# Performance work log

Measured on AMD Instinct MI355X. Metric: run time of the kernel, lower is better.

## Reference

```python
import jax, jax.numpy as jnp
import numpy as np
from jax.scipy.special import logsumexp

DEPTH = 7
LOG_EPS = jnp.float32(-64.0)
EPS = jnp.float32(np.exp(-64.0))


def leaf_interval(depth, start_idx=0):
    if depth == 0:
        return ([start_idx], [start_idx], [], start_idx)
    l_l, l_r, l_adj, last = leaf_interval(depth - 1, start_idx)
    my = last + 1
    r_l, r_r, r_adj, last = leaf_interval(depth - 1, my + 1)
    return ([my] + l_l, [my] + r_r,
            [(l, r) for l in l_r for r in r_l] + l_adj + r_adj, last)


_start, _end, _adj, _ = leaf_interval(DEPTH)
_out_idx = np.array([i for i, _ in _adj], dtype=np.int32)
OUT_UNIQ, OUT_INV = np.unique(_out_idx, return_inverse=True)
IN_IDX = np.array([j for _, j in _adj], dtype=np.int32)
START_IDXS = np.array(_start, dtype=np.int32)
END_IDXS = np.array(_end, dtype=np.int32)
N_STATES = 2 ** (DEPTH + 1) - 1  # 255


def log_safe(x):
    m = x < EPS
    return jnp.where(m, LOG_EPS, jnp.log(jnp.where(m, EPS, x)))


def exp_safe(x):
    m = x < LOG_EPS
    return jnp.where(m, EPS, jnp.exp(jnp.where(m, LOG_EPS, x)))


def setup_inputs() -> dict:
    key = jax.random.key(0)
    k1, k2, k3 = jax.random.split(key, 3)
    V, B, vocab, T = N_STATES, 64, 5000, 50
    log_probs = jax.nn.log_softmax(
        jax.random.normal(k1, (V, B, vocab), dtype=jnp.float32), axis=-1)
    targets = jax.random.randint(k2, (T, B), 0, vocab)
    target_lengths = jax.random.randint(k3, (B,), 1, T + 1)
    return {"log_probs": log_probs, "targets": targets,
            "target_lengths": target_lengths}


def _forward_ctreec(extracted, target_lengths):
    # extracted: [T, B, V] time-major per-state label log-probs
    T, B, V = extracted.shape
    out_uniq = jnp.asarray(OUT_UNIQ)
    out_inv = jnp.asarray(OUT_INV)
    in_idx = jnp.asarray(IN_IDX)
    end_idxs = jnp.asarray(END_IDXS)
    prev0 = jnp.zeros((B, V), jnp.float32).at[:, jnp.asarray(START_IDXS)].set(1.0)
    acc0 = jnp.zeros((B,), jnp.float32)

    def step(carry, xs):
        prev_probs, acc = carry
        elp_t, t = xs
        log_curr = log_safe(prev_probs) + elp_t            # [B, V]
        log_out = log_curr[:, out_uniq]                    # [B, U] unique out nodes
        log_C = logsumexp(log_out, axis=-1, keepdims=True)  # [B, 1]
        outgoing = exp_safe(log_out - log_C)[:, out_inv]   # [B, E] per-edge probs
        end = (t + 1) == target_lengths                    # [B]
        end_vals = logsumexp(log_curr[:, end_idxs], axis=1)
        acc = acc + jnp.where(end, end_vals, 0.0)
        mid = ((t + 1) < target_lengths) & (t < T - 1)
        acc = acc + jnp.where(mid, log_C[:, 0], 0.0)
        # scatter-add outgoing edge mass onto destination nodes
        new_prev = jnp.zeros_like(prev_probs).at[:, in_idx].add(outgoing)
        return (new_prev, acc), None

    (_, acc), _ = jax.lax.scan(step, (prev0, acc0),
                               (extracted, jnp.arange(T)))
    return acc


def reference(log_probs, targets, target_lengths):
    V, B, vocab = log_probs.shape
    # extracted[t, b, v] = log_probs[v, b, targets[t, b]]
    extracted = log_probs[:, jnp.arange(B)[None, :], targets]  # [V, T, B]
    extracted = jnp.transpose(extracted, (1, 2, 0))            # [T, B, V]
    return -_forward_ctreec(extracted, target_lengths)
```

## Files before the change

kernel.cpp:

```cpp
#include <hip/hip_runtime.h>
#include <math.h>


#define TT 50
#define BB 64
#define VOCAB 5000
#define NS 255
#define NSP 256
#define LOG_EPS_F (-64.0f)
#define EPS_F 1.6038109389511818e-28f
#define WS_NEEDED ((size_t)BB * TT * NSP * 4)

__device__ __forceinline__ float wred_max(float x) {
#pragma unroll
    for (int m = 32; m >= 1; m >>= 1) x = fmaxf(x, __shfl_xor(x, m));
    return x;
}
__device__ __forceinline__ float wred_sum(float x) {
#pragma unroll
    for (int m = 32; m >= 1; m >>= 1) x += __shfl_xor(x, m);
    return x;
}

__global__ __launch_bounds__(256) void gather_kernel(
    const float* __restrict__ log_probs,
    const int* __restrict__ targets,
    const int* __restrict__ target_lengths,
    float* __restrict__ ews)
{
    const int bt = blockIdx.x;
    const int b = bt / TT;
    const int t = bt % TT;
    if (t >= target_lengths[b]) return;
    const int v = threadIdx.x;
    const int tgt = targets[t * BB + b];
    float val = -1e30f;
    if (v < NS)
        val = log_probs[(size_t)v * (BB * VOCAB) + (size_t)b * VOCAB + tgt];
    ews[(size_t)bt * NSP + v] = val;
}

__global__ __launch_bounds__(64) void scan_kernel(
    const float* __restrict__ ews,
    const int* __restrict__ target_lengths,
    float* __restrict__ out)
{
    const int b = blockIdx.x;
    const int lane = threadIdx.x;
    const int vbase = lane * 4;
    __shared__ float outv[NSP];

    const int len = target_lengths[b];
    const float4* ew = (const float4*)(ews + (size_t)b * TT * NSP);

    bool isend[4], isout[4];
    int kk[4], jj[4];
    float prev[4];
#pragma unroll
    for (int i = 0; i < 4; ++i) {
        int v = vbase + i;
        int p = v + 1;
        bool valid = (v < NS);
        bool pw2 = (p & (p - 1)) == 0;
        bool e_ = valid && ((p + (p & (-p))) == 256);
        isend[i] = e_;
        isout[i] = valid && !e_;
        prev[i] = (valid && pw2) ? 1.0f : 0.0f;
        if (valid && !pw2) {
            int s = __ffs(p) - 1;
            int q = p & (p - 1);
            kk[i] = __ffs(q) - 1;
            jj[i] = v - (1 << s);
        } else { kk[i] = 0; jj[i] = 0; }
    }

    float acc = 0.0f;
    float4 e4 = ew[lane];
    for (int t = 0; t < len; ++t) {
        float4 cur = e4;
        if (t + 1 < len) e4 = ew[(t + 1) * 64 + lane];

        float lc[4];
#pragma unroll
        for (int i = 0; i < 4; ++i) {
            float pv = prev[i];
            float lp = (pv < EPS_F) ? LOG_EPS_F : __logf(pv);
            lc[i] = lp + ((const float*)&cur)[i];
        }

        if (t == len - 1) {
            float m = -INFINITY;
#pragma unroll
            for (int i = 0; i < 4; ++i)
                if (isend[i]) m = fmaxf(m, lc[i]);
            m = wred_max(m);
            float s = 0.0f;
#pragma unroll
            for (int i = 0; i < 4; ++i)
                if (isend[i]) s += __expf(lc[i] - m);
            s = wred_sum(s);
            acc += m + __logf(s);
        } else {
            float m = -INFINITY;
#pragma unroll
            for (int i = 0; i < 4; ++i)
                if (isout[i]) m = fmaxf(m, lc[i]);
            m = wred_max(m);
            float s = 0.0f;
#pragma unroll
            for (int i = 0; i < 4; ++i)
                if (isout[i]) s += __expf(lc[i] - m);
            s = wred_sum(s);
            float logC = m + __logf(s);
            acc += logC;

#pragma unroll
            for (int i = 0; i < 4; ++i) {
                float d = lc[i] - logC;
                outv[vbase + i] = (d < LOG_EPS_F) ? EPS_F : __expf(d);
            }
            __syncthreads();
#pragma unroll
            for (int i = 0; i < 4; ++i) {
                float np_ = 0.0f;
                int bj = jj[i];
                int n = kk[i];
                for (int a = 0; a < n; ++a) np_ += outv[bj - (1 << a)];
                prev[i] = np_;
            }
            __syncthreads();
        }
    }
    if (lane == 0) out[b] = -acc;
}

__global__ __launch_bounds__(64) void ctreec_fused(
    const float* __restrict__ log_probs,
    const int* __restrict__ targets,
    const int* __restrict__ target_lengths,
    float* __restrict__ out)
{
    const int b = blockIdx.x;
    const int lane = threadIdx.x;
    const int vbase = lane * 4;
    __shared__ float e_lds[TT * NSP];
    __shared__ float outv[NSP];
    __shared__ int tgts[TT];
    const int len = target_lengths[b];
    if (lane < TT) tgts[lane] = targets[lane * BB + b];
    __syncthreads();
    {
        const size_t bvoff = (size_t)b * VOCAB;
        float4* e_vec = (float4*)e_lds;
#pragma unroll 4
        for (int t = 0; t < len; ++t) {
            const float* base = log_probs + bvoff + (size_t)tgts[t];
            float4 val;
            val.x = base[(size_t)(vbase + 0) * (BB * VOCAB)];
            val.y = base[(size_t)(vbase + 1) * (BB * VOCAB)];
            val.z = base[(size_t)(vbase + 2) * (BB * VOCAB)];
            val.w = (vbase + 3 < NS) ? base[(size_t)(vbase + 3) * (BB * VOCAB)] : -1e30f;
            e_vec[t * 64 + lane] = val;
        }
    }
    __syncthreads();
    bool isend[4], isout[4];
    int kk[4], jj[4];
    float prev[4];
#pragma unroll
    for (int i = 0; i < 4; ++i) {
        int v = vbase + i;
        int p = v + 1;
        bool valid = (v < NS);
        bool pw2 = (p & (p - 1)) == 0;
        bool e_ = valid && ((p + (p & (-p))) == 256);
        isend[i] = e_;
        isout[i] = valid && !e_;
        prev[i] = (valid && pw2) ? 1.0f : 0.0f;
        if (valid && !pw2) {
            int s = __ffs(p) - 1;
            int q = p & (p - 1);
            kk[i] = __ffs(q) - 1;
            jj[i] = v - (1 << s);
        } else { kk[i] = 0; jj[i] = 0; }
    }
    const float4* e_vec = (const float4*)e_lds;
    float acc = 0.0f;
    for (int t = 0; t < len; ++t) {
        float4 e4 = e_vec[t * 64 + lane];
        float e[4] = {e4.x, e4.y, e4.z, e4.w};
        float lc[4];
#pragma unroll
        for (int i = 0; i < 4; ++i) {
            float pv = prev[i];
            float lp = (pv < EPS_F) ? LOG_EPS_F : __logf(pv);
            lc[i] = lp + e[i];
        }
        if (t == len - 1) {
            float m = -INFINITY;
#pragma unroll
            for (int i = 0; i < 4; ++i)
                if (isend[i]) m = fmaxf(m, lc[i]);
            m = wred_max(m);
            float s = 0.0f;
#pragma unroll
            for (int i = 0; i < 4; ++i)
                if (isend[i]) s += __expf(lc[i] - m);
            s = wred_sum(s);
            acc += m + __logf(s);
        } else {
            float m = -INFINITY;
#pragma unroll
            for (int i = 0; i < 4; ++i)
                if (isout[i]) m = fmaxf(m, lc[i]);
            m = wred_max(m);
            float s = 0.0f;
#pragma unroll
            for (int i = 0; i < 4; ++i)
                if (isout[i]) s += __expf(lc[i] - m);
            s = wred_sum(s);
            float logC = m + __logf(s);
            acc += logC;
#pragma unroll
            for (int i = 0; i < 4; ++i) {
                float d = lc[i] - logC;
                outv[vbase + i] = (d < LOG_EPS_F) ? EPS_F : __expf(d);
            }
            __syncthreads();
#pragma unroll
            for (int i = 0; i < 4; ++i) {
                float np_ = 0.0f;
                int bj = jj[i];
                int n = kk[i];
                for (int a = 0; a < n; ++a) np_ += outv[bj - (1 << a)];
                prev[i] = np_;
            }
            __syncthreads();
        }
    }
    if (lane == 0) out[b] = -acc;
}

extern "C" void kernel_launch(void* const* d_in, const int* in_sizes, int n_in,
                              void* d_out, int out_size, void* d_ws, size_t ws_size,
                              hipStream_t stream) {
    const float* log_probs = (const float*)d_in[0];
    const int* targets = (const int*)d_in[1];
    const int* target_lengths = (const int*)d_in[2];
    float* out = (float*)d_out;

    if (ws_size >= WS_NEEDED) {
        float* ews = (float*)d_ws;
        gather_kernel<<<dim3(BB * TT), dim3(256), 0, stream>>>(
            log_probs, targets, target_lengths, ews);
        scan_kernel<<<dim3(BB), dim3(64), 0, stream>>>(
            ews, target_lengths, out);
    } else {
        ctreec_fused<<<dim3(BB), dim3(64), 0, stream>>>(
            log_probs, targets, target_lengths, out);
    }
}
```

Before: 460.7 us.

## Run CTreeC scan in linear probability space with exp done in gather

The per-step log/exp work in the serial scan is replaced by linear-space products. The gather kernel now stores exp(log_prob), so the scan multiplies prev by the emission, sums, and normalizes by a reciprocal of the sum, dropping the max-reduction and the per-element exp and log. The second global load is also prefetched two steps ahead. This removes the safe-log/exp clamping at EPS, so results can differ or underflow in extreme cases (e.g. all emissions very small giving a zero sum).

```diff
diff --git a/kernel.cpp b/kernel.cpp
--- a/kernel.cpp
+++ b/kernel.cpp
@@ -11,14 +11,14 @@
 #define EPS_F 1.6038109389511818e-28f
 #define WS_NEEDED ((size_t)BB * TT * NSP * 4)
 
+__device__ __forceinline__ float wred_sum(float x) {
+#pragma unroll
+    for (int m = 32; m >= 1; m >>= 1) x += __shfl_xor(x, m);
+    return x;
+}
 __device__ __forceinline__ float wred_max(float x) {
 #pragma unroll
     for (int m = 32; m >= 1; m >>= 1) x = fmaxf(x, __shfl_xor(x, m));
-    return x;
-}
-__device__ __forceinline__ float wred_sum(float x) {
-#pragma unroll
-    for (int m = 32; m >= 1; m >>= 1) x += __shfl_xor(x, m);
     return x;
 }
 
@@ -34,9 +34,9 @@
     if (t >= target_lengths[b]) return;
     const int v = threadIdx.x;
     const int tgt = targets[t * BB + b];
-    float val = -1e30f;
+    float val = 0.0f;
     if (v < NS)
-        val = log_probs[(size_t)v * (BB * VOCAB) + (size_t)b * VOCAB + tgt];
+        val = __expf(log_probs[(size_t)v * (BB * VOCAB) + (size_t)b * VOCAB + tgt]);
     ews[(size_t)bt * NSP + v] = val;
 }
 
@@ -75,50 +75,35 @@
     }
 
     float acc = 0.0f;
-    float4 e4 = ew[lane];
+    float4 eA = ew[lane];
+    float4 eB = (len > 1) ? ew[64 + lane] : eA;
     for (int t = 0; t < len; ++t) {
-        float4 cur = e4;
-        if (t + 1 < len) e4 = ew[(t + 1) * 64 + lane];
-
-        float lc[4];
-#pragma unroll
-        for (int i = 0; i < 4; ++i) {
-            float pv = prev[i];
-            float lp = (pv < EPS_F) ? LOG_EPS_F : __logf(pv);
-            lc[i] = lp + ((const float*)&cur)[i];
-        }
+        float4 cur = eA;
+        eA = eB;
+        if (t + 2 < len) eB = ew[(t + 2) * 64 + lane];
+
+        float c[4];
+        c[0] = prev[0] * cur.x;
+        c[1] = prev[1] * cur.y;
+        c[2] = prev[2] * cur.z;
+        c[3] = prev[3] * cur.w;
 
         if (t == len - 1) {
-            float m = -INFINITY;
-#pragma unroll
-            for (int i = 0; i < 4; ++i)
-                if (isend[i]) m = fmaxf(m, lc[i]);
-            m = wred_max(m);
-            float s = 0.0f;
-#pragma unroll
-            for (int i = 0; i < 4; ++i)
-                if (isend[i]) s += __expf(lc[i] - m);
-            s = wred_sum(s);
-            acc += m + __logf(s);
+            float s = 0.0f;
+#pragma unroll
+            for (int i = 0; i < 4; ++i)
+                if (isend[i]) s += c[i];
+            s = wred_sum(s);
+            acc += __logf(s);
         } else {
-            float m = -INFINITY;
-#pragma unroll
-            for (int i = 0; i < 4; ++i)
-                if (isout[i]) m = fmaxf(m, lc[i]);
-            m = wred_max(m);
-            float s = 0.0f;
-#pragma unroll
-            for (int i = 0; i < 4; ++i)
-                if (isout[i]) s += __expf(lc[i] - m);
-            s = wred_sum(s);
-            float logC = m + __logf(s);
-            acc += logC;
-
-#pragma unroll
-            for (int i = 0; i < 4; ++i) {
-                float d = lc[i] - logC;
-                outv[vbase + i] = (d < LOG_EPS_F) ? EPS_F : __expf(d);
-            }
+            *(float4*)&outv[vbase] = make_float4(c[0], c[1], c[2], c[3]);
+            float s = 0.0f;
+#pragma unroll
+            for (int i = 0; i < 4; ++i)
+                if (isout[i]) s += c[i];
+            s = wred_sum(s);
+            acc += __logf(s);
+            float rinv = 1.0f / s;
             __syncthreads();
 #pragma unroll
             for (int i = 0; i < 4; ++i) {
@@ -126,7 +111,7 @@
                 int bj = jj[i];
                 int n = kk[i];
                 for (int a = 0; a < n; ++a) np_ += outv[bj - (1 << a)];
-                prev[i] = np_;
+                prev[i] = np_ * rinv;
             }
             __syncthreads();
         }
```

After: 441.6 us. 1.04x faster.
